# Optimization experiments

Hardware: AMD Instinct MI355X
Metric: run time of the kernel (lower is better)

## Reference

```python
import jax, jax.numpy as jnp
import numpy as np

H = 128   # render_height
W = 128   # render_width
N = 128   # primitives per frame (from view(B,128,12,2))
K = 12    # control points / polygon vertices per primitive
SOFT = 0.01  # fallback_softness of DiffRasterizer


def setup_inputs() -> dict:
    key = jax.random.key(0)
    k1, k2, k3, k4, k5 = jax.random.split(key, 5)
    T, B = 192, 1
    # state = [3072 control-point coords in [0,1] | 128 aliveness logits]
    trajectory = jax.random.uniform(k1, (T, B, N * K * 2 + N), dtype=jnp.float32)
    colors = jax.random.uniform(k2, (B, N, 3), dtype=jnp.float32)
    alpha = jax.random.uniform(k3, (N,), dtype=jnp.float32)
    z = jax.random.normal(k4, (N,), dtype=jnp.float32)
    csg = jax.random.randint(k5, (N,), 0, 2) > 0
    return {"trajectory": trajectory, "colors": colors, "alpha": alpha, "z": z, "csg": csg}


def _raster(P, c, alpha, alive, z, csg, gx, gy):
    """Soft differentiable rasterizer (fallback path).
    P: [N,K,2] polygon control points in [0,1]; c: [N,3]; alpha/alive/z: [N]; csg: [N] bool.
    Coverage: product of per-edge half-plane sigmoids (soft convex polygon),
    orientation-corrected via shoelace sign. Composited back-to-front by z;
    CSG-subtract primitives erase (occlude) without contributing color.
    """
    v0 = P                                   # [N,K,2]
    v1 = jnp.roll(P, -1, axis=1)             # [N,K,2]
    e = v1 - v0                              # edge vectors
    area2 = jnp.sum(v0[..., 0] * v1[..., 1] - v1[..., 0] * v0[..., 1], axis=1)  # [N]
    orient = jax.lax.stop_gradient(jnp.sign(area2))[:, None]                    # [N,1]
    # signed edge tests for every pixel: [H,W,N,K]
    s = e[..., 0] * (gy[:, :, None, None] - v0[..., 1]) \
      - e[..., 1] * (gx[:, :, None, None] - v0[..., 0])
    cov = jnp.prod(jax.nn.sigmoid(s * orient / SOFT), axis=-1)  # [H,W,N]
    a = cov * alpha * jax.nn.sigmoid(alive)                     # per-primitive alpha
    order = jnp.argsort(z)                                      # back-to-front
    a = a[..., order]
    c = c[order]
    sub = csg[order].astype(a.dtype)
    one_m = 1.0 - a
    # exclusive reverse cumulative transmittance T_i = prod_{j>i}(1 - a_j)
    t_acc = jnp.flip(jnp.cumprod(jnp.flip(one_m, -1), -1), -1)
    t_excl = jnp.concatenate([t_acc[..., 1:], jnp.ones_like(t_acc[..., :1])], -1)
    w = a * t_excl * (1.0 - sub)             # [H,W,N]
    return jnp.einsum('hwn,nc->hwc', w, c)   # [H,W,3]


def reference(trajectory, colors, alpha, z, csg):
    T, B, _ = trajectory.shape
    ys = (jnp.arange(H, dtype=jnp.float32) + 0.5) / H
    xs = (jnp.arange(W, dtype=jnp.float32) + 0.5) / W
    gy, gx = jnp.meshgrid(ys, xs, indexing='ij')  # [H,W]

    def frame(state_t):  # state_t: [B, 3200]
        P = state_t[:, :N * K * 2].reshape(B, N, K, 2)
        alive = state_t[:, N * K * 2:].reshape(B, N)
        return jax.vmap(lambda Pb, cb, ab: _raster(Pb, cb, alpha, ab, z, csg, gx, gy))(P, colors, alive)

    video = jax.lax.map(jax.checkpoint(frame), trajectory)  # [T,B,H,W,3]
    return jnp.transpose(video, (1, 0, 2, 3, 4))            # [B,T,H,W,3]
```

## Files before the change

### kernel.cpp

```cpp
#include <hip/hip_runtime.h>


#define HH 128
#define WW 128
#define NN 128
#define KK 12
#define STPB 1024
#define RTPB 256
#define STATE_SZ (NN * KK * 2 + NN)
#define CULL_U 15.0f
#define COEF_STRIDE 40

typedef float f2 __attribute__((ext_vector_type(2)));

__global__ __launch_bounds__(STPB) void setup_kernel(
    const float* __restrict__ traj,
    const float* __restrict__ colors,
    const float* __restrict__ alpha,
    const float* __restrict__ zval,
    const void*  __restrict__ csg_raw,
    float* __restrict__ g_coef,
    int* __restrict__ g_cnt,
    unsigned char* __restrict__ g_list)
{
    __shared__ __align__(16) float s_coef[NN][COEF_STRIDE];
    __shared__ __align__(16) float2 s_pq[NN][KK];
    __shared__ float s_state[STATE_SZ];
    __shared__ float s_orient[NN];
    __shared__ float s_z[NN];
    __shared__ int   s_slot2prim[NN];
    __shared__ int   s_npos[NN], s_nneg[NN];
    __shared__ unsigned long long s_qbits[HH][4][2];
    __shared__ unsigned char s_list[4 * (HH / 2)][NN];
    __shared__ int s_cnt[4 * (HH / 2)];
    __shared__ int s_mode;

    const int frame = blockIdx.x;
    const int tid   = threadIdx.x;
    const float* st = traj + (size_t)frame * STATE_SZ;

    for (int i = tid; i < STATE_SZ; i += STPB) s_state[i] = st[i];
    if (tid < NN) { s_z[tid] = zval[tid]; s_npos[tid] = 0; s_nneg[tid] = 0; }
    if (tid == 0) {
        const unsigned char* b = (const unsigned char*)csg_raw;
        const unsigned int*  w = (const unsigned int*)csg_raw;
        int mode = 0;
        bool words01 = true;
        for (int i = 0; i < 32; i++) if (w[i] > 1u) { words01 = false; break; }
        if (!words01) {
            bool bytes01 = true;
            for (int i = 0; i < 128; i++) if (b[i] > 1) { bytes01 = false; break; }
            mode = bytes01 ? 1 : 2;
        }
        s_mode = mode;
    }
    __syncthreads();

    if (tid < NN) {
        const int n = tid;
        float area2 = 0.f;
        #pragma unroll
        for (int k = 0; k < KK; k++) {
            int k1 = (k + 1) % KK;
            float v0x = s_state[(n * KK + k)  * 2 + 0];
            float v0y = s_state[(n * KK + k)  * 2 + 1];
            float v1x = s_state[(n * KK + k1) * 2 + 0];
            float v1y = s_state[(n * KK + k1) * 2 + 1];
            area2 += v0x * v1y - v1x * v0y;
        }
        float orient = (area2 > 0.f) ? 1.f : ((area2 < 0.f) ? -1.f : 0.f);
        s_orient[n] = orient;

        float alive = s_state[NN * KK * 2 + n];
        float g = alpha[n] / (1.f + __expf(-alive));

        float zn = s_z[n];
        int rank = 0;
        for (int j = 0; j < NN; j++) {
            float zj = s_z[j];
            rank += (zj < zn || (zj == zn && j < n)) ? 1 : 0;
        }
        int slot = (NN - 1) - rank;
        s_slot2prim[slot] = n;

        int mode = s_mode;
        int sub;
        if (mode == 0)      sub = ((const int*)csg_raw)[n] != 0;
        else if (mode == 1) sub = ((const unsigned char*)csg_raw)[n] != 0;
        else                sub = ((const float*)csg_raw)[n] != 0.f;
        float cs = sub ? 0.f : 1.f;
        s_coef[slot][36] = g;
        s_coef[slot][37] = colors[n * 3 + 0] * cs;
        s_coef[slot][38] = colors[n * 3 + 1] * cs;
        s_coef[slot][39] = colors[n * 3 + 2] * cs;
    }
    __syncthreads();

    const float QSCALE = 100.0f * 1.4426950408889634f;
    for (int idx = tid; idx < NN * KK; idx += STPB) {
        int slot = idx / KK;
        int k    = idx - slot * KK;
        int n    = s_slot2prim[slot];
        int k1   = (k + 1) % KK;
        float v0x = s_state[(n * KK + k)  * 2 + 0];
        float v0y = s_state[(n * KK + k)  * 2 + 1];
        float v1x = s_state[(n * KK + k1) * 2 + 0];
        float v1y = s_state[(n * KK + k1) * 2 + 1];
        float ex = v1x - v0x, ey = v1y - v0y;
        float q  = -s_orient[n] * QSCALE;
        s_coef[slot][0  + k] = q * ex;
        s_coef[slot][12 + k] = -q * ey;
        s_coef[slot][24 + k] = -q * (ex * v0y - ey * v0x);
    }
    __syncthreads();

    const float SLACK = 0.01f;
    for (int idx = tid; idx < NN * KK; idx += STPB) {
        int slot = idx / KK;
        int k    = idx - slot * KK;
        (void)k;
        float A = s_coef[slot][idx - slot * KK];
        float B = s_coef[slot][12 + (idx - slot * KK)];
        float C = s_coef[slot][24 + (idx - slot * KK)];
        float rcpB = __builtin_amdgcn_rcpf(B);
        float Praw = (CULL_U - C) * rcpB;
        float Qraw = -A * rcpB;
        if (B > 0.f) {
            int i = atomicAdd(&s_npos[slot], 1);
            s_pq[slot][i] = make_float2(Qraw, Praw + SLACK);
        } else if (B < 0.f) {
            int i = atomicAdd(&s_nneg[slot], 1);
            s_pq[slot][(KK - 1) - i] = make_float2(-Qraw, -Praw + SLACK);
        } else {
            int i = atomicAdd(&s_nneg[slot], 1);
            s_pq[slot][(KK - 1) - i] = make_float2(0.f, 1e30f);
        }
    }
    __syncthreads();

    const float GX_LO = 0.5f / WW;
    const float GX_HI = (WW - 0.5f) / WW;
    for (int j = 0; j < (HH * NN) / STPB; j++) {
        int idx = j * STPB + tid;
        int r = idx >> 7, s = idx & (NN - 1);
        float gyr = (r + 0.5f) * (1.0f / HH);
        int npos = s_npos[s];
        const float4* pq4 = (const float4*)&s_pq[s][0];
        float y1 = 1e30f, y2 = 1e30f;
        #pragma unroll
        for (int h = 0; h < KK / 2; h++) {
            float4 v = pq4[h];
            int k0 = 2 * h, k1 = 2 * h + 1;
            float t0 = fmaf(v.x, gyr, v.y);
            float t1 = fmaf(v.z, gyr, v.w);
            bool p0 = k0 < npos, p1 = k1 < npos;
            y1 = fminf(y1, p0 ? t0 : 1e30f);
            y2 = fminf(y2, p0 ? 1e30f : t0);
            y1 = fminf(y1, p1 ? t1 : 1e30f);
            y2 = fminf(y2, p1 ? 1e30f : t1);
        }
        float xhi = fminf(y1, GX_HI);
        float xlo = fmaxf(-y2, GX_LO);
        bool ne = (xlo <= xhi);
        #pragma unroll
        for (int q = 0; q < 4; q++) {
            float qlo = (q * 32 + 0.5f) * (1.0f / WW);
            float qhi = (q * 32 + 31.5f) * (1.0f / WW);
            unsigned long long m = __ballot(ne && (xlo <= qhi) && (xhi >= qlo));
            if ((tid & 63) == 0) s_qbits[r][q][(s >= 64) ? 1 : 0] = m;
        }
    }
    __syncthreads();

    if (tid < 4 * (HH / 2)) {
        int rp = tid >> 2, q = tid & 3;
        unsigned long long b0 = s_qbits[2 * rp][q][0] | s_qbits[2 * rp + 1][q][0];
        unsigned long long b1 = s_qbits[2 * rp][q][1] | s_qbits[2 * rp + 1][q][1];
        int n = 0;
        while (b0) { int k = __builtin_ctzll(b0); b0 &= b0 - 1; s_list[tid][n++] = (unsigned char)k; }
        while (b1) { int k = __builtin_ctzll(b1); b1 &= b1 - 1; s_list[tid][n++] = (unsigned char)(64 + k); }
        s_cnt[tid] = n;
    }
    __syncthreads();

    {
        float* dstc = g_coef + (size_t)frame * (NN * COEF_STRIDE);
        const float* srcc = &s_coef[0][0];
        for (int i = tid; i < NN * COEF_STRIDE; i += STPB) dstc[i] = srcc[i];
        if (tid < 256) g_cnt[frame * 256 + tid] = s_cnt[tid];
        unsigned int* dstl = (unsigned int*)(g_list + (size_t)frame * (256 * NN));
        const unsigned int* srcl = (const unsigned int*)&s_list[0][0];
        for (int i = tid; i < (256 * NN) / 4; i += STPB) dstl[i] = srcl[i];
    }
}

struct F3 { float x, y, z; };

__global__ __launch_bounds__(RTPB) void raster_kernel(
    const float* __restrict__ g_coef,
    const int* __restrict__ g_cnt,
    const unsigned char* __restrict__ g_list,
    float* __restrict__ out)
{
    __shared__ unsigned char s_wlist[4][NN];

    const int tid   = threadIdx.x;
    const int wv    = __builtin_amdgcn_readfirstlane(tid >> 6);
    const int lane  = tid & 63;
    const int frame = blockIdx.y;
    const int tile  = blockIdx.x * 4 + wv;
    const int rp    = tile >> 2;
    const int q     = tile & 3;

    const unsigned char* lst = g_list + ((size_t)frame * 256 + tile) * NN;
    if (lane < NN / 4) {
        ((unsigned int*)&s_wlist[wv][0])[lane] = ((const unsigned int*)lst)[lane];
    }
    const int cnt = g_cnt[frame * 256 + tile];

    const int lx  = lane & 31, ly = lane >> 5;
    const int px  = q * 32 + lx;
    const int row = rp * 2 + ly;
    const float gy = (row + 0.5f) * (1.0f / HH);
    const float gx = (px  + 0.5f) * (1.0f / WW);
    const f2 gy2 = {gy, gy};
    const f2 gx2 = {gx, gx};
    const f2 lo2 = {-100.f, -100.f};

    const float* cfr = g_coef + (size_t)frame * (NN * COEF_STRIDE);

    float Tt = 1.f, rr = 0.f, gg = 0.f, bb = 0.f;
    for (int i = 0; i < cnt; i++) {
        int slot = __builtin_amdgcn_readfirstlane((int)s_wlist[wv][i]);
        const float* cf = cfr + slot * COEF_STRIDE;
        const f2* A2 = (const f2*)(cf);
        const f2* B2 = (const f2*)(cf + 12);
        const f2* C2 = (const f2*)(cf + 24);

        f2 qv = {1.f, 1.f};
        #pragma unroll
        for (int j = 0; j < 6; j++) {
            f2 u = __builtin_elementwise_fma(B2[j], gx2,
                     __builtin_elementwise_fma(A2[j], gy2, C2[j]));
            u = __builtin_elementwise_max(u, lo2);
            f2 e;
            e.x = __builtin_amdgcn_exp2f(u.x);
            e.y = __builtin_amdgcn_exp2f(u.y);
            qv = __builtin_elementwise_fma(qv, e, qv);
        }
        float cov = __builtin_amdgcn_rcpf(qv.x * qv.y);

        float a = cov * cf[36];
        float w = a * Tt;
        rr = fmaf(w, cf[37], rr);
        gg = fmaf(w, cf[38], gg);
        bb = fmaf(w, cf[39], bb);
        Tt = fmaf(-a, Tt, Tt);

        if (!__any(Tt > 2e-3f)) break;
    }

    size_t o = ((size_t)frame * (HH * WW) + (size_t)row * WW + px) * 3;
    *(F3*)(out + o) = F3{rr, gg, bb};
}

extern "C" void kernel_launch(void* const* d_in, const int* in_sizes, int n_in,
                              void* d_out, int out_size, void* d_ws, size_t ws_size,
                              hipStream_t stream) {
    const float* traj   = (const float*)d_in[0];
    const float* colors = (const float*)d_in[1];
    const float* alpha  = (const float*)d_in[2];
    const float* zval   = (const float*)d_in[3];
    const void*  csg    = d_in[4];
    float* out = (float*)d_out;

    const int T = in_sizes[0] / STATE_SZ;

    size_t coef_sz = (size_t)T * NN * COEF_STRIDE * sizeof(float);
    size_t cnt_sz  = (size_t)T * 256 * sizeof(int);
    float* g_coef = (float*)d_ws;
    int*   g_cnt  = (int*)((char*)d_ws + coef_sz);
    unsigned char* g_list = (unsigned char*)d_ws + coef_sz + cnt_sz;

    setup_kernel<<<T, STPB, 0, stream>>>(traj, colors, alpha, zval, csg,
                                         g_coef, g_cnt, g_list);
    dim3 grid(256 / 4, T);
    raster_kernel<<<grid, RTPB, 0, stream>>>(g_coef, g_cnt, g_list, out);
}
```

Before: 208.4 us.

## Prefetch next primitive coefficients, parallelize list build and csg mode detection

The raster loop now software-pipelines coefficient loads, fetching the next primitive's 40 floats while computing the current one to hide global/scalar load latency. The setup kernel replaces the single-thread csg dtype scan with wave ballots, replaces the serial per-tile bit-to-list loop with a wave-parallel mbcnt compaction, pads the s_pq shared array, and unrolls the z-rank loop. These reduce serial thread work in setup and load latency in raster, at the cost of more registers in the raster loop.

```diff
diff --git a/kernel.cpp b/kernel.cpp
--- a/kernel.cpp
+++ b/kernel.cpp
@@ -10,6 +10,7 @@
 #define STATE_SZ (NN * KK * 2 + NN)
 #define CULL_U 15.0f
 #define COEF_STRIDE 40
+#define PQ_STRIDE 18
 
 typedef float f2 __attribute__((ext_vector_type(2)));
 
@@ -24,7 +25,7 @@
     unsigned char* __restrict__ g_list)
 {
     __shared__ __align__(16) float s_coef[NN][COEF_STRIDE];
-    __shared__ __align__(16) float2 s_pq[NN][KK];
+    __shared__ __align__(16) float2 s_pq[NN][PQ_STRIDE];
     __shared__ float s_state[STATE_SZ];
     __shared__ float s_orient[NN];
     __shared__ float s_z[NN];
@@ -41,18 +42,11 @@
 
     for (int i = tid; i < STATE_SZ; i += STPB) s_state[i] = st[i];
     if (tid < NN) { s_z[tid] = zval[tid]; s_npos[tid] = 0; s_nneg[tid] = 0; }
-    if (tid == 0) {
-        const unsigned char* b = (const unsigned char*)csg_raw;
-        const unsigned int*  w = (const unsigned int*)csg_raw;
-        int mode = 0;
-        bool words01 = true;
-        for (int i = 0; i < 32; i++) if (w[i] > 1u) { words01 = false; break; }
-        if (!words01) {
-            bool bytes01 = true;
-            for (int i = 0; i < 128; i++) if (b[i] > 1) { bytes01 = false; break; }
-            mode = bytes01 ? 1 : 2;
-        }
-        s_mode = mode;
+    if (tid < 64) {
+        unsigned w = (tid < 32) ? ((const unsigned*)csg_raw)[tid] : 0u;
+        unsigned long long anyw = __ballot(w > 1u);
+        unsigned long long anyb = __ballot((w & 0xFEFEFEFEu) != 0u);
+        if (tid == 0) s_mode = (anyw == 0ull) ? 0 : ((anyb == 0ull) ? 1 : 2);
     }
     __syncthreads();
 
@@ -76,6 +70,7 @@
 
         float zn = s_z[n];
         int rank = 0;
+        #pragma unroll 8
         for (int j = 0; j < NN; j++) {
             float zj = s_z[j];
             rank += (zj < zn || (zj == zn && j < n)) ? 1 : 0;
@@ -172,14 +167,23 @@
     }
     __syncthreads();
 
-    if (tid < 4 * (HH / 2)) {
-        int rp = tid >> 2, q = tid & 3;
-        unsigned long long b0 = s_qbits[2 * rp][q][0] | s_qbits[2 * rp + 1][q][0];
-        unsigned long long b1 = s_qbits[2 * rp][q][1] | s_qbits[2 * rp + 1][q][1];
-        int n = 0;
-        while (b0) { int k = __builtin_ctzll(b0); b0 &= b0 - 1; s_list[tid][n++] = (unsigned char)k; }
-        while (b1) { int k = __builtin_ctzll(b1); b1 &= b1 - 1; s_list[tid][n++] = (unsigned char)(64 + k); }
-        s_cnt[tid] = n;
+    {
+        int wvS = tid >> 6;
+        int ln  = tid & 63;
+        for (int it = 0; it < 16; it++) {
+            int t = wvS * 16 + it;
+            int rp = t >> 2, qq = t & 3;
+            unsigned long long b0 = s_qbits[2 * rp][qq][0] | s_qbits[2 * rp + 1][qq][0];
+            unsigned long long b1 = s_qbits[2 * rp][qq][1] | s_qbits[2 * rp + 1][qq][1];
+            int c0 = __popcll(b0);
+            int p0 = __builtin_amdgcn_mbcnt_hi((unsigned)(b0 >> 32),
+                     __builtin_amdgcn_mbcnt_lo((unsigned)b0, 0));
+            int p1 = __builtin_amdgcn_mbcnt_hi((unsigned)(b1 >> 32),
+                     __builtin_amdgcn_mbcnt_lo((unsigned)b1, 0));
+            if ((b0 >> ln) & 1ull) s_list[t][p0]      = (unsigned char)ln;
+            if ((b1 >> ln) & 1ull) s_list[t][c0 + p1] = (unsigned char)(64 + ln);
+            if (ln == 0) s_cnt[t] = c0 + __popcll(b1);
+        }
     }
     __syncthreads();
 
@@ -230,34 +234,56 @@
     const float* cfr = g_coef + (size_t)frame * (NN * COEF_STRIDE);
 
     float Tt = 1.f, rr = 0.f, gg = 0.f, bb = 0.f;
-    for (int i = 0; i < cnt; i++) {
-        int slot = __builtin_amdgcn_readfirstlane((int)s_wlist[wv][i]);
-        const float* cf = cfr + slot * COEF_STRIDE;
-        const f2* A2 = (const f2*)(cf);
-        const f2* B2 = (const f2*)(cf + 12);
-        const f2* C2 = (const f2*)(cf + 24);
-
-        f2 qv = {1.f, 1.f};
+    if (cnt > 0) {
+        int sl_n = __builtin_amdgcn_readfirstlane((int)s_wlist[wv][0]);
+        const float* cfn = cfr + sl_n * COEF_STRIDE;
+        f2 An[6], Bn[6], Cn[6]; float4 gcn;
         #pragma unroll
         for (int j = 0; j < 6; j++) {
-            f2 u = __builtin_elementwise_fma(B2[j], gx2,
-                     __builtin_elementwise_fma(A2[j], gy2, C2[j]));
-            u = __builtin_elementwise_max(u, lo2);
-            f2 e;
-            e.x = __builtin_amdgcn_exp2f(u.x);
-            e.y = __builtin_amdgcn_exp2f(u.y);
-            qv = __builtin_elementwise_fma(qv, e, qv);
-        }
-        float cov = __builtin_amdgcn_rcpf(qv.x * qv.y);
-
-        float a = cov * cf[36];
-        float w = a * Tt;
-        rr = fmaf(w, cf[37], rr);
-        gg = fmaf(w, cf[38], gg);
-        bb = fmaf(w, cf[39], bb);
-        Tt = fmaf(-a, Tt, Tt);
-
-        if (!__any(Tt > 2e-3f)) break;
+            An[j] = ((const f2*)(cfn     ))[j];
+            Bn[j] = ((const f2*)(cfn + 12))[j];
+            Cn[j] = ((const f2*)(cfn + 24))[j];
+        }
+        gcn = *(const float4*)(cfn + 36);
+
+        for (int i = 0; i < cnt; i++) {
+            f2 A[6], B[6], C[6]; float4 gc = gcn;
+            #pragma unroll
+            for (int j = 0; j < 6; j++) { A[j] = An[j]; B[j] = Bn[j]; C[j] = Cn[j]; }
+
+            int inx = (i + 1 < cnt) ? (i + 1) : i;
+            sl_n = __builtin_amdgcn_readfirstlane((int)s_wlist[wv][inx]);
+            cfn = cfr + sl_n * COEF_STRIDE;
+            #pragma unroll
+            for (int j = 0; j < 6; j++) {
+                An[j] = ((const f2*)(cfn     ))[j];
+                Bn[j] = ((const f2*)(cfn + 12))[j];
+                Cn[j] = ((const f2*)(cfn + 24))[j];
+            }
+            gcn = *(const float4*)(cfn + 36);
+
+            f2 qv = {1.f, 1.f};
+            #pragma unroll
+            for (int j = 0; j < 6; j++) {
+                f2 u = __builtin_elementwise_fma(B[j], gx2,
+                         __builtin_elementwise_fma(A[j], gy2, C[j]));
+                u = __builtin_elementwise_max(u, lo2);
+                f2 e;
+                e.x = __builtin_amdgcn_exp2f(u.x);
+                e.y = __builtin_amdgcn_exp2f(u.y);
+                qv = __builtin_elementwise_fma(qv, e, qv);
+            }
+            float cov = __builtin_amdgcn_rcpf(qv.x * qv.y);
+
+            float a = cov * gc.x;
+            float w = a * Tt;
+            rr = fmaf(w, gc.y, rr);
+            gg = fmaf(w, gc.z, gg);
+            bb = fmaf(w, gc.w, bb);
+            Tt = fmaf(-a, Tt, Tt);
+
+            if (!__any(Tt > 2e-3f)) break;
+        }
     }
 
     size_t o = ((size_t)frame * (HH * WW) + (size_t)row * WW + px) * 3;
```

Result: slower. 228.0 us (+9.4%).
